# Kernel tuning notes

Hardware: AMD Instinct MI355X
Metric: run time of the kernel (lower is better)

## Reference

```python
import jax, jax.numpy as jnp
import numpy as np

N_NODES = 50000
N_EDGES = 400000
NODE_DIM = 128
NUM_BASIS = 20
MUL0, MUL1, MUL2 = 128, 64, 32          # 128x0e + 64x1e + 32x2e
NUM_IRREPS = MUL0 + MUL1 + MUL2         # 224
SPH_DIM = MUL0 + 3 * MUL1 + 5 * MUL2    # 480
HIDDEN = NODE_DIM + NUM_IRREPS          # 352
EPS = 1e-5


def layer_norm(x, g, b):
    mu = x.mean(-1, keepdims=True)
    var = ((x - mu) ** 2).mean(-1, keepdims=True)
    return (x - mu) * jax.lax.rsqrt(var + EPS) * g + b


def o3_layer_norm(x, w, b):
    # Equivariant layer norm per irrep block (Equiformer-style, component normalization).
    s = x[:, :MUL0]                                    # l=0 scalars [N,128]
    v = x[:, MUL0:MUL0 + 3 * MUL1].reshape(-1, MUL1, 3)  # l=1 [N,64,3]
    t = x[:, MUL0 + 3 * MUL1:].reshape(-1, MUL2, 5)      # l=2 [N,32,5]
    s = s - s.mean(-1, keepdims=True)
    s = s * jax.lax.rsqrt((s ** 2).mean(-1, keepdims=True) + EPS) * w[:MUL0] + b
    nv = (v ** 2).mean(axis=(-1, -2))[:, None, None]
    v = v * jax.lax.rsqrt(nv + EPS) * w[MUL0:MUL0 + MUL1][None, :, None]
    nt = (t ** 2).mean(axis=(-1, -2))[:, None, None]
    t = t * jax.lax.rsqrt(nt + EPS) * w[MUL0 + MUL1:][None, :, None]
    return jnp.concatenate([s, v.reshape(-1, 3 * MUL1), t.reshape(-1, 5 * MUL2)], axis=-1)


def sph_harm(vec):
    # e3nn spherical harmonics (normalize=True, normalization='component') up to l=2.
    u = vec * jax.lax.rsqrt((vec ** 2).sum(-1, keepdims=True))
    x, y, z = u[:, 0], u[:, 1], u[:, 2]
    s15 = np.float32(np.sqrt(15.0))
    s5 = np.float32(np.sqrt(5.0))
    sh1 = np.float32(np.sqrt(3.0)) * u  # [E,3]
    sh2 = jnp.stack([s15 * x * z,
                     s15 * x * y,
                     s5 * (y * y - 0.5 * (x * x + z * z)),
                     s15 * y * z,
                     0.5 * s15 * (z * z - x * x)], axis=-1)  # [E,5]
    return sh1, sh2


def _forward(x_scalar, x_spherical, rbf, vec, W1, b1, W2, b2, Wrbf, ln_g, ln_b, o3_w, o3_b, edge_index):
    dst, src = edge_index[0], edge_index[1]
    scalar_in = layer_norm(x_scalar, ln_g, ln_b)          # [N,128]
    spherical_in = o3_layer_norm(x_spherical, o3_w, o3_b)  # [N,480]
    h = jax.nn.silu(scalar_in @ W1 + b1)
    scalar_out = h @ W2 + b2                               # [N,352]
    filter_weight = rbf @ Wrbf                             # [E,352]
    filter_out = scalar_out[src] * filter_weight           # gather + elementwise [E,352]
    gate = filter_out[:, :NUM_IRREPS]                      # [E,224]
    message_scalar = filter_out[:, NUM_IRREPS:]            # [E,128]
    sh1, sh2 = sph_harm(vec)
    g0 = gate[:, :MUL0]
    g1 = gate[:, MUL0:MUL0 + MUL1]
    g2 = gate[:, MUL0 + MUL1:]
    # ElementwiseTensorProduct(edge_irreps, '224x0e'): scalar gate per irrep; l=0 SH == 1.
    msg1 = (g1[:, :, None] * sh1[:, None, :]).reshape(-1, 3 * MUL1)
    msg2 = (g2[:, :, None] * sh2[:, None, :]).reshape(-1, 5 * MUL2)
    message_spherical = jnp.concatenate([g0, msg1, msg2], axis=-1)  # [E,480]
    new_scalar = scalar_in.at[dst].add(message_scalar)
    new_spherical = spherical_in.at[dst].add(message_spherical)
    return new_scalar, new_spherical


def setup_inputs() -> dict:
    key = jax.random.key(0)
    ks = jax.random.split(key, 8)
    return {
        "x_scalar": jax.random.normal(ks[0], (N_NODES, NODE_DIM), dtype=jnp.float32),
        "x_spherical": jax.random.normal(ks[1], (N_NODES, SPH_DIM), dtype=jnp.float32),
        "rbf": jax.random.normal(ks[2], (N_EDGES, NUM_BASIS), dtype=jnp.float32),
        "vec": jax.random.normal(ks[3], (N_EDGES, 3), dtype=jnp.float32),
        "W1": jax.random.normal(ks[4], (NODE_DIM, NODE_DIM), dtype=jnp.float32) * 0.05,
        "b1": jnp.zeros((NODE_DIM,), jnp.float32),
        "W2": jax.random.normal(ks[5], (NODE_DIM, HIDDEN), dtype=jnp.float32) * 0.05,
        "b2": jnp.zeros((HIDDEN,), jnp.float32),
        "Wrbf": jax.random.normal(ks[6], (NUM_BASIS, HIDDEN), dtype=jnp.float32) * 0.05,
        "ln_g": jnp.ones((NODE_DIM,), jnp.float32),
        "ln_b": jnp.zeros((NODE_DIM,), jnp.float32),
        "o3_w": jnp.ones((NUM_IRREPS,), jnp.float32),
        "o3_b": jnp.zeros((MUL0,), jnp.float32),
        "edge_index": jax.random.randint(ks[7], (2, N_EDGES), 0, N_NODES),
    }


def reference(x_scalar, x_spherical, rbf, vec, W1, b1, W2, b2, Wrbf, ln_g, ln_b, o3_w, o3_b, edge_index):
    return _forward(x_scalar, x_spherical, rbf, vec, W1, b1, W2, b2, Wrbf, ln_g, ln_b, o3_w, o3_b, edge_index)
```

## Files before the change

### kernel.cpp

```cpp
#include <hip/hip_runtime.h>
#include <hip/hip_bf16.h>

#define N_DIM   128
#define MUL0    128
#define MUL1    64
#define MUL2    32
#define NIRR    224
#define SPHD    480
#define HID     352
#define NBASIS  20
#define EPSV    1e-5f

typedef __attribute__((ext_vector_type(8))) short bf16x8;
typedef __attribute__((ext_vector_type(4))) float f32x4;

__device__ __forceinline__ float wave_sum(float v) {
  #pragma unroll
  for (int o = 32; o > 0; o >>= 1) v += __shfl_xor(v, o, 64);
  return v;
}

__device__ __forceinline__ unsigned short f2bf(float f) {
  unsigned int u = __float_as_uint(f);
  u = (u + 0x7fff + ((u >> 16) & 1)) >> 16;
  return (unsigned short)u;
}

__global__ __launch_bounds__(256) void node_norm_kernel(
    const float* __restrict__ x_scalar, const float* __restrict__ x_sph,
    const float* __restrict__ ln_g, const float* __restrict__ ln_b,
    const float* __restrict__ o3_w, const float* __restrict__ o3_b,
    float* __restrict__ out_scal, float* __restrict__ out_sph, int n_nodes) {
  const int n = blockIdx.x * 4 + (threadIdx.x >> 6);
  if (n >= n_nodes) return;
  const int l = threadIdx.x & 63;

  const float* xs = x_scalar + (size_t)n * N_DIM;
  float a0 = xs[l], a1 = xs[l + 64];
  float mu = wave_sum(a0 + a1) * (1.f / 128.f);
  float d0 = a0 - mu, d1 = a1 - mu;
  float var = wave_sum(d0 * d0 + d1 * d1) * (1.f / 128.f);
  float sc = rsqrtf(var + EPSV);
  float* os = out_scal + (size_t)n * N_DIM;
  os[l]      = d0 * sc * ln_g[l]      + ln_b[l];
  os[l + 64] = d1 * sc * ln_g[l + 64] + ln_b[l + 64];

  const float* xp = x_sph + (size_t)n * SPHD;
  float s0 = xp[l], s1 = xp[l + 64];
  mu = wave_sum(s0 + s1) * (1.f / 128.f);
  d0 = s0 - mu; d1 = s1 - mu;
  var = wave_sum(d0 * d0 + d1 * d1) * (1.f / 128.f);
  sc = rsqrtf(var + EPSV);
  float* op = out_sph + (size_t)n * SPHD;
  op[l]      = d0 * sc * o3_w[l]      + o3_b[l];
  op[l + 64] = d1 * sc * o3_w[l + 64] + o3_b[l + 64];

  float v0 = xp[128 + l], v1 = xp[128 + 64 + l], v2 = xp[128 + 128 + l];
  float nv = wave_sum(v0 * v0 + v1 * v1 + v2 * v2) * (1.f / 192.f);
  sc = rsqrtf(nv + EPSV);
  op[128 + l]       = v0 * sc * o3_w[MUL0 + (l) / 3];
  op[128 + 64 + l]  = v1 * sc * o3_w[MUL0 + (l + 64) / 3];
  op[128 + 128 + l] = v2 * sc * o3_w[MUL0 + (l + 128) / 3];

  float t0 = xp[320 + l], t1 = xp[320 + 64 + l];
  float t2 = (l < 32) ? xp[320 + 128 + l] : 0.f;
  float nt = wave_sum(t0 * t0 + t1 * t1 + t2 * t2) * (1.f / 160.f);
  sc = rsqrtf(nt + EPSV);
  op[320 + l]      = t0 * sc * o3_w[MUL0 + MUL1 + (l) / 5];
  op[320 + 64 + l] = t1 * sc * o3_w[MUL0 + MUL1 + (l + 64) / 5];
  if (l < 32) op[320 + 128 + l] = t2 * sc * o3_w[MUL0 + MUL1 + (l + 128) / 5];
}

__global__ void pack_b_kernel(const float* __restrict__ B, unsigned short* __restrict__ Bp,
                              int N, int NT) {
  int id = blockIdx.x * 256 + threadIdx.x;
  int total = 4 * NT * 64;
  if (id >= total) return;
  int lane = id & 63;
  int tmp = id >> 6;
  int nt = tmp % NT, ks = tmp / NT;
  int n = nt * 16 + (lane & 15);
  int kb = ks * 32 + (lane >> 4) * 8;
  unsigned short* o = Bp + (size_t)id * 8;
  #pragma unroll
  for (int j = 0; j < 8; ++j)
    o[j] = (n < N) ? f2bf(B[(size_t)(kb + j) * N + n]) : (unsigned short)0;
}

template <bool A_BF16, bool SILU, bool OUT_BF16>
__global__ __launch_bounds__(256) void mfma_gemm_kernel(
    const void* __restrict__ Ap, const unsigned short* __restrict__ Bp,
    const float* __restrict__ bias, void* __restrict__ Cp,
    int M, int N, int NT) {
  const int lane = threadIdx.x & 63;
  const int wave = threadIdx.x >> 6;
  const int bm = blockIdx.x * 64 + wave * 16;
  const int bn = blockIdx.y * 64;
  const int q = lane >> 4;
  const int arow = min(bm + (lane & 15), M - 1);

  f32x4 acc[4] = {};
  #pragma unroll
  for (int ks = 0; ks < 4; ++ks) {
    const int k = ks * 32 + q * 8;
    bf16x8 a;
    if (A_BF16) {
      a = *(const bf16x8*)((const unsigned short*)Ap + (size_t)arow * 128 + k);
    } else {
      const float* ap = (const float*)Ap + (size_t)arow * 128 + k;
      float4 f0 = *(const float4*)ap;
      float4 f1 = *(const float4*)(ap + 4);
      union { bf16x8 v; unsigned short s[8]; } cv;
      cv.s[0] = f2bf(f0.x); cv.s[1] = f2bf(f0.y); cv.s[2] = f2bf(f0.z); cv.s[3] = f2bf(f0.w);
      cv.s[4] = f2bf(f1.x); cv.s[5] = f2bf(f1.y); cv.s[6] = f2bf(f1.z); cv.s[7] = f2bf(f1.w);
      a = cv.v;
    }
    #pragma unroll
    for (int nt = 0; nt < 4; ++nt) {
      bf16x8 b = *(const bf16x8*)(Bp + ((size_t)(ks * NT + blockIdx.y * 4 + nt) * 64 + lane) * 8);
      acc[nt] = __builtin_amdgcn_mfma_f32_16x16x32_bf16(a, b, acc[nt], 0, 0, 0);
    }
  }
  #pragma unroll
  for (int nt = 0; nt < 4; ++nt) {
    int col = bn + nt * 16 + (lane & 15);
    if (col >= N) continue;
    float bz = bias[col];
    #pragma unroll
    for (int i = 0; i < 4; ++i) {
      int r = bm + q * 4 + i;
      if (r >= M) continue;
      float v = acc[nt][i] + bz;
      if (SILU) v = v / (1.f + __expf(-v));
      if (OUT_BF16) ((unsigned short*)Cp)[(size_t)r * N + col] = f2bf(v);
      else          ((float*)Cp)[(size_t)r * N + col] = v;
    }
  }
}

__global__ void hist_kernel(const int* __restrict__ ei, int* __restrict__ deg, int n_edges) {
  int e = blockIdx.x * blockDim.x + threadIdx.x;
  if (e < n_edges) atomicAdd(&deg[ei[e]], 1);
}

__global__ __launch_bounds__(1024) void scan_part_kernel(
    const int* __restrict__ deg, int* __restrict__ offs, int* __restrict__ bsum, int n) {
  __shared__ int wsum[16];
  const int tid = threadIdx.x, lane = tid & 63, wid = tid >> 6;
  int i = blockIdx.x * 1024 + tid;
  int v = (i < n) ? deg[i] : 0;
  int s = v;
  #pragma unroll
  for (int o = 1; o < 64; o <<= 1) {
    int t = __shfl_up(s, o, 64);
    if (lane >= o) s += t;
  }
  if (lane == 63) wsum[wid] = s;
  __syncthreads();
  if (wid == 0) {
    int ws = (lane < 16) ? wsum[lane] : 0;
    #pragma unroll
    for (int o = 1; o < 16; o <<= 1) {
      int t = __shfl_up(ws, o, 64);
      if (lane >= o) ws += t;
    }
    if (lane < 16) wsum[lane] = ws;
  }
  __syncthreads();
  int excl = ((wid == 0) ? 0 : wsum[wid - 1]) + s - v;
  if (i < n) offs[i] = excl;
  if (tid == 1023) bsum[blockIdx.x] = wsum[15];
}

__global__ __launch_bounds__(64) void scan_tops_kernel(
    const int* __restrict__ bsum, int* __restrict__ bbase, int* __restrict__ offs,
    int nb, int n) {
  const int lane = threadIdx.x;
  int v = (lane < nb) ? bsum[lane] : 0;
  int s = v;
  #pragma unroll
  for (int o = 1; o < 64; o <<= 1) {
    int t = __shfl_up(s, o, 64);
    if (lane >= o) s += t;
  }
  if (lane < nb) bbase[lane] = s - v;
  if (lane == 63) offs[n] = s;
}

__global__ __launch_bounds__(1024) void scan_add_kernel(
    int* __restrict__ offs, const int* __restrict__ bbase, int n) {
  int i = blockIdx.x * 1024 + threadIdx.x;
  if (i < n) offs[i] += bbase[blockIdx.x];
}

__global__ void fill_kernel(const int* __restrict__ ei, const int* __restrict__ offs,
                            int* __restrict__ cursor, const int* __restrict__ edge_src,
                            const float* __restrict__ rbf, const float* __restrict__ vec,
                            float* __restrict__ rbf_s, float* __restrict__ vec_s,
                            int* __restrict__ src_s, int n_edges) {
  int e = blockIdx.x * blockDim.x + threadIdx.x;
  if (e < n_edges) {
    int d = ei[e];
    int p = atomicAdd(&cursor[d], 1);
    int ii = offs[d] + p;
    src_s[ii] = edge_src[e];
    const float4* rp = (const float4*)(rbf + (size_t)e * NBASIS);
    float4* op = (float4*)(rbf_s + (size_t)ii * NBASIS);
    op[0] = rp[0]; op[1] = rp[1]; op[2] = rp[2]; op[3] = rp[3]; op[4] = rp[4];
    vec_s[(size_t)ii * 3]     = vec[(size_t)e * 3];
    vec_s[(size_t)ii * 3 + 1] = vec[(size_t)e * 3 + 1];
    vec_s[(size_t)ii * 3 + 2] = vec[(size_t)e * 3 + 2];
  }
}

#define NPB 4
#define S3f  1.7320508075688772f
#define S15f 3.872983346207417f
#define S5f  2.2360679774997896f

__device__ __forceinline__ void edge_accum(
    int ii, float sA, float sB,
    const float* __restrict__ rbf_s, const float* __restrict__ vec_s,
    const float* wA, const float* wB, int t, bool hasB,
    float& a0, float& a1, float& a2, float& a3, float& a4, float& aB) {
  const float4* rp = (const float4*)(rbf_s + (size_t)ii * NBASIS);
  float4 r0 = rp[0], r1 = rp[1], r2 = rp[2], r3 = rp[3], r4 = rp[4];
  float rb[NBASIS] = {r0.x, r0.y, r0.z, r0.w, r1.x, r1.y, r1.z, r1.w,
                      r2.x, r2.y, r2.z, r2.w, r3.x, r3.y, r3.z, r3.w,
                      r4.x, r4.y, r4.z, r4.w};
  float fwA = 0.f;
  #pragma unroll
  for (int k = 0; k < NBASIS; ++k) fwA += rb[k] * wA[k];
  float fA = sA * fwA;

  if (t < 128) {
    a0 += fA;
  } else if (t < 224) {
    float vx = vec_s[3 * (size_t)ii], vy = vec_s[3 * (size_t)ii + 1], vz = vec_s[3 * (size_t)ii + 2];
    float rn = rsqrtf(vx * vx + vy * vy + vz * vz);
    float x = vx * rn, y = vy * rn, z = vz * rn;
    if (t < 192) {
      a0 += fA * (S3f * x); a1 += fA * (S3f * y); a2 += fA * (S3f * z);
    } else {
      a0 += fA * (S15f * x * z);
      a1 += fA * (S15f * x * y);
      a2 += fA * (S5f * (y * y - 0.5f * (x * x + z * z)));
      a3 += fA * (S15f * y * z);
      a4 += fA * (0.5f * S15f * (z * z - x * x));
    }
  } else {
    a0 += fA;
  }

  if (hasB) {
    float fwB = 0.f;
    #pragma unroll
    for (int k = 0; k < NBASIS; ++k) fwB += rb[k] * wB[k];
    aB += sB * fwB;
  }
}

__global__ __launch_bounds__(256) void gather_kernel(
    const float* __restrict__ rbf_s, const float* __restrict__ vec_s,
    const float* __restrict__ Wrbf, const float* __restrict__ so,
    const int* __restrict__ src_s, const int* __restrict__ offs,
    float* __restrict__ out_scal, float* __restrict__ out_sph, int n_nodes) {
  const int t = threadIdx.x;
  const bool hasB = (t < 96);
  const int cA = t;
  const int cB = hasB ? (256 + t) : 256;

  float wA[NBASIS], wB[NBASIS];
  #pragma unroll
  for (int k = 0; k < NBASIS; ++k) {
    wA[k] = Wrbf[k * HID + cA];
    wB[k] = Wrbf[k * HID + cB];
  }

  const int nb = blockIdx.x * NPB;
  for (int nn = 0; nn < NPB; ++nn) {
    const int node = nb + nn;
    if (node >= n_nodes) break;
    float a0 = 0.f, a1 = 0.f, a2 = 0.f, a3 = 0.f, a4 = 0.f, aB = 0.f;
    const int e0 = offs[node], e1 = offs[node + 1];

    int ii = e0;
    for (; ii + 4 <= e1; ii += 4) {
      const int s0 = src_s[ii], s1 = src_s[ii + 1], s2 = src_s[ii + 2], s3 = src_s[ii + 3];
      const float* p0 = so + (size_t)s0 * HID;
      const float* p1 = so + (size_t)s1 * HID;
      const float* p2 = so + (size_t)s2 * HID;
      const float* p3 = so + (size_t)s3 * HID;
      float sA0 = p0[cA], sA1 = p1[cA], sA2 = p2[cA], sA3 = p3[cA];
      float sB0 = hasB ? p0[cB] : 0.f;
      float sB1 = hasB ? p1[cB] : 0.f;
      float sB2 = hasB ? p2[cB] : 0.f;
      float sB3 = hasB ? p3[cB] : 0.f;
      edge_accum(ii,     sA0, sB0, rbf_s, vec_s, wA, wB, t, hasB, a0, a1, a2, a3, a4, aB);
      edge_accum(ii + 1, sA1, sB1, rbf_s, vec_s, wA, wB, t, hasB, a0, a1, a2, a3, a4, aB);
      edge_accum(ii + 2, sA2, sB2, rbf_s, vec_s, wA, wB, t, hasB, a0, a1, a2, a3, a4, aB);
      edge_accum(ii + 3, sA3, sB3, rbf_s, vec_s, wA, wB, t, hasB, a0, a1, a2, a3, a4, aB);
    }
    for (; ii + 2 <= e1; ii += 2) {
      const int s0 = src_s[ii], s1 = src_s[ii + 1];
      const float* p0 = so + (size_t)s0 * HID;
      const float* p1 = so + (size_t)s1 * HID;
      float sA0 = p0[cA], sA1 = p1[cA];
      float sB0 = hasB ? p0[cB] : 0.f;
      float sB1 = hasB ? p1[cB] : 0.f;
      edge_accum(ii,     sA0, sB0, rbf_s, vec_s, wA, wB, t, hasB, a0, a1, a2, a3, a4, aB);
      edge_accum(ii + 1, sA1, sB1, rbf_s, vec_s, wA, wB, t, hasB, a0, a1, a2, a3, a4, aB);
    }
    if (ii < e1) {
      const int s0 = src_s[ii];
      const float* p0 = so + (size_t)s0 * HID;
      float sA0 = p0[cA];
      float sB0 = hasB ? p0[cB] : 0.f;
      edge_accum(ii, sA0, sB0, rbf_s, vec_s, wA, wB, t, hasB, a0, a1, a2, a3, a4, aB);
    }

    float* sph = out_sph + (size_t)node * SPHD;
    float* scl = out_scal + (size_t)node * N_DIM;
    if (t < 128) {
      sph[t] += a0;
    } else if (t < 192) {
      float* p = sph + 128 + 3 * (t - 128);
      p[0] += a0; p[1] += a1; p[2] += a2;
    } else if (t < 224) {
      float* p = sph + 320 + 5 * (t - 192);
      p[0] += a0; p[1] += a1; p[2] += a2; p[3] += a3; p[4] += a4;
    } else {
      scl[t - 224] += a0;
    }
    if (hasB) scl[t + 32] += aB;
  }
}

extern "C" void kernel_launch(void* const* d_in, const int* in_sizes, int n_in,
                              void* d_out, int out_size, void* d_ws, size_t ws_size,
                              hipStream_t stream) {
  const float* x_scalar = (const float*)d_in[0];
  const float* x_sph    = (const float*)d_in[1];
  const float* rbf      = (const float*)d_in[2];
  const float* vec      = (const float*)d_in[3];
  const float* W1       = (const float*)d_in[4];
  const float* b1       = (const float*)d_in[5];
  const float* W2       = (const float*)d_in[6];
  const float* b2       = (const float*)d_in[7];
  const float* Wrbf     = (const float*)d_in[8];
  const float* ln_g     = (const float*)d_in[9];
  const float* ln_b     = (const float*)d_in[10];
  const float* o3_w     = (const float*)d_in[11];
  const float* o3_b     = (const float*)d_in[12];
  const int*   edge_idx = (const int*)d_in[13];

  const int n_nodes = in_sizes[0] / N_DIM;
  const int n_edges = in_sizes[2] / NBASIS;

  float* out_scal = (float*)d_out;
  float* out_sph  = out_scal + (size_t)n_nodes * N_DIM;

  float* rbf_s = (float*)d_ws;
  float* vec_s = rbf_s + (size_t)n_edges * NBASIS;
  int*   src_s = (int*)(vec_s + (size_t)n_edges * 3);
  float* ws_so = (float*)(src_s + n_edges);
  unsigned short* h_bf = (unsigned short*)(ws_so + (size_t)n_nodes * HID);
  unsigned short* bp1  = h_bf + (size_t)n_nodes * N_DIM;
  unsigned short* bp2  = bp1 + 16384;
  int* deg    = (int*)(bp2 + 49152);
  int* cursor = deg + n_nodes;
  int* offs   = cursor + n_nodes;
  int* bsum   = offs + n_nodes + 1;
  int* bbase  = bsum + 64;

  const int* edge_dst = edge_idx;
  const int* edge_src = edge_idx + n_edges;

  node_norm_kernel<<<(n_nodes + 3) / 4, 256, 0, stream>>>(
      x_scalar, x_sph, ln_g, ln_b, o3_w, o3_b, out_scal, out_sph, n_nodes);

  pack_b_kernel<<<8, 256, 0, stream>>>(W1, bp1, N_DIM, 8);
  pack_b_kernel<<<24, 256, 0, stream>>>(W2, bp2, HID, 24);

  {
    dim3 g((n_nodes + 63) / 64, 2);
    mfma_gemm_kernel<false, true, true><<<g, 256, 0, stream>>>(
        out_scal, bp1, b1, h_bf, n_nodes, N_DIM, 8);
  }
  {
    dim3 g((n_nodes + 63) / 64, 6);
    mfma_gemm_kernel<true, false, false><<<g, 256, 0, stream>>>(
        h_bf, bp2, b2, ws_so, n_nodes, HID, 24);
  }

  hipMemsetAsync(deg, 0, sizeof(int) * 2 * n_nodes, stream);
  hist_kernel<<<(n_edges + 255) / 256, 256, 0, stream>>>(edge_dst, deg, n_edges);
  const int nb = (n_nodes + 1023) / 1024;
  scan_part_kernel<<<nb, 1024, 0, stream>>>(deg, offs, bsum, n_nodes);
  scan_tops_kernel<<<1, 64, 0, stream>>>(bsum, bbase, offs, nb, n_nodes);
  scan_add_kernel<<<nb, 1024, 0, stream>>>(offs, bbase, n_nodes);
  fill_kernel<<<(n_edges + 255) / 256, 256, 0, stream>>>(
      edge_dst, offs, cursor, edge_src, rbf, vec, rbf_s, vec_s, src_s, n_edges);

  gather_kernel<<<(n_nodes + NPB - 1) / NPB, 256, 0, stream>>>(
      rbf_s, vec_s, Wrbf, ws_so, src_s, offs, out_scal, out_sph, n_nodes);
}
```

Before: 676.4 us.

## Store scalar_out in bf16 with interleaved column layout for gather

```diff
diff --git a/kernel.cpp b/kernel.cpp
--- a/kernel.cpp
+++ b/kernel.cpp
@@ -24,6 +24,10 @@
   unsigned int u = __float_as_uint(f);
   u = (u + 0x7fff + ((u >> 16) & 1)) >> 16;
   return (unsigned short)u;
+}
+
+__device__ __forceinline__ float bf2f(unsigned short v) {
+  return __uint_as_float(((unsigned int)v) << 16);
 }
 
 __global__ __launch_bounds__(256) void node_norm_kernel(
@@ -87,7 +91,7 @@
     o[j] = (n < N) ? f2bf(B[(size_t)(kb + j) * N + n]) : (unsigned short)0;
 }
 
-template <bool A_BF16, bool SILU, bool OUT_BF16>
+template <bool A_BF16, bool SILU, bool OUT_BF16, bool PERM>
 __global__ __launch_bounds__(256) void mfma_gemm_kernel(
     const void* __restrict__ Ap, const unsigned short* __restrict__ Bp,
     const float* __restrict__ bias, void* __restrict__ Cp,
@@ -126,14 +130,16 @@
     int col = bn + nt * 16 + (lane & 15);
     if (col >= N) continue;
     float bz = bias[col];
+    int pcol = col;
+    if (PERM) pcol = (col < 96) ? (2 * col) : ((col < 256) ? (col + 96) : (2 * (col - 256) + 1));
     #pragma unroll
     for (int i = 0; i < 4; ++i) {
       int r = bm + q * 4 + i;
       if (r >= M) continue;
       float v = acc[nt][i] + bz;
       if (SILU) v = v / (1.f + __expf(-v));
-      if (OUT_BF16) ((unsigned short*)Cp)[(size_t)r * N + col] = f2bf(v);
-      else          ((float*)Cp)[(size_t)r * N + col] = v;
+      if (OUT_BF16) ((unsigned short*)Cp)[(size_t)r * N + pcol] = f2bf(v);
+      else          ((float*)Cp)[(size_t)r * N + pcol] = v;
     }
   }
 }
@@ -218,6 +224,20 @@
 #define S15f 3.872983346207417f
 #define S5f  2.2360679774997896f
 
+__device__ __forceinline__ void so_load(const unsigned short* __restrict__ so,
+                                        int src, int t, bool hasB,
+                                        float& sA, float& sB) {
+  const unsigned short* p = so + (size_t)src * HID;
+  if (hasB) {
+    unsigned int u = *(const unsigned int*)(p + 2 * t);
+    sA = __uint_as_float(u << 16);
+    sB = __uint_as_float(u & 0xffff0000u);
+  } else {
+    sA = bf2f(p[t + 96]);
+    sB = 0.f;
+  }
+}
+
 __device__ __forceinline__ void edge_accum(
     int ii, float sA, float sB,
     const float* __restrict__ rbf_s, const float* __restrict__ vec_s,
@@ -262,7 +282,7 @@
 
 __global__ __launch_bounds__(256) void gather_kernel(
     const float* __restrict__ rbf_s, const float* __restrict__ vec_s,
-    const float* __restrict__ Wrbf, const float* __restrict__ so,
+    const float* __restrict__ Wrbf, const unsigned short* __restrict__ so,
     const int* __restrict__ src_s, const int* __restrict__ offs,
     float* __restrict__ out_scal, float* __restrict__ out_sph, int n_nodes) {
   const int t = threadIdx.x;
@@ -287,15 +307,11 @@
     int ii = e0;
     for (; ii + 4 <= e1; ii += 4) {
       const int s0 = src_s[ii], s1 = src_s[ii + 1], s2 = src_s[ii + 2], s3 = src_s[ii + 3];
-      const float* p0 = so + (size_t)s0 * HID;
-      const float* p1 = so + (size_t)s1 * HID;
-      const float* p2 = so + (size_t)s2 * HID;
-      const float* p3 = so + (size_t)s3 * HID;
-      float sA0 = p0[cA], sA1 = p1[cA], sA2 = p2[cA], sA3 = p3[cA];
-      float sB0 = hasB ? p0[cB] : 0.f;
-      float sB1 = hasB ? p1[cB] : 0.f;
-      float sB2 = hasB ? p2[cB] : 0.f;
-      float sB3 = hasB ? p3[cB] : 0.f;
+      float sA0, sB0, sA1, sB1, sA2, sB2, sA3, sB3;
+      so_load(so, s0, t, hasB, sA0, sB0);
+      so_load(so, s1, t, hasB, sA1, sB1);
+      so_load(so, s2, t, hasB, sA2, sB2);
+      so_load(so, s3, t, hasB, sA3, sB3);
       edge_accum(ii,     sA0, sB0, rbf_s, vec_s, wA, wB, t, hasB, a0, a1, a2, a3, a4, aB);
       edge_accum(ii + 1, sA1, sB1, rbf_s, vec_s, wA, wB, t, hasB, a0, a1, a2, a3, a4, aB);
       edge_accum(ii + 2, sA2, sB2, rbf_s, vec_s, wA, wB, t, hasB, a0, a1, a2, a3, a4, aB);
@@ -303,19 +319,16 @@
     }
     for (; ii + 2 <= e1; ii += 2) {
       const int s0 = src_s[ii], s1 = src_s[ii + 1];
-      const float* p0 = so + (size_t)s0 * HID;
-      const float* p1 = so + (size_t)s1 * HID;
-      float sA0 = p0[cA], sA1 = p1[cA];
-      float sB0 = hasB ? p0[cB] : 0.f;
-      float sB1 = hasB ? p1[cB] : 0.f;
+      float sA0, sB0, sA1, sB1;
+      so_load(so, s0, t, hasB, sA0, sB0);
+      so_load(so, s1, t, hasB, sA1, sB1);
       edge_accum(ii,     sA0, sB0, rbf_s, vec_s, wA, wB, t, hasB, a0, a1, a2, a3, a4, aB);
       edge_accum(ii + 1, sA1, sB1, rbf_s, vec_s, wA, wB, t, hasB, a0, a1, a2, a3, a4, aB);
     }
     if (ii < e1) {
       const int s0 = src_s[ii];
-      const float* p0 = so + (size_t)s0 * HID;
-      float sA0 = p0[cA];
-      float sB0 = hasB ? p0[cB] : 0.f;
+      float sA0, sB0;
+      so_load(so, s0, t, hasB, sA0, sB0);
       edge_accum(ii, sA0, sB0, rbf_s, vec_s, wA, wB, t, hasB, a0, a1, a2, a3, a4, aB);
     }
 
@@ -363,10 +376,10 @@
   float* rbf_s = (float*)d_ws;
   float* vec_s = rbf_s + (size_t)n_edges * NBASIS;
   int*   src_s = (int*)(vec_s + (size_t)n_edges * 3);
-  float* ws_so = (float*)(src_s + n_edges);
-  unsigned short* h_bf = (unsigned short*)(ws_so + (size_t)n_nodes * HID);
-  unsigned short* bp1  = h_bf + (size_t)n_nodes * N_DIM;
-  unsigned short* bp2  = bp1 + 16384;
+  unsigned short* so_bf = (unsigned short*)(src_s + n_edges);
+  unsigned short* h_bf  = so_bf + (size_t)n_nodes * HID;
+  unsigned short* bp1   = h_bf + (size_t)n_nodes * N_DIM;
+  unsigned short* bp2   = bp1 + 16384;
   int* deg    = (int*)(bp2 + 49152);
   int* cursor = deg + n_nodes;
   int* offs   = cursor + n_nodes;
@@ -384,13 +397,13 @@
 
   {
     dim3 g((n_nodes + 63) / 64, 2);
-    mfma_gemm_kernel<false, true, true><<<g, 256, 0, stream>>>(
+    mfma_gemm_kernel<false, true, true, false><<<g, 256, 0, stream>>>(
         out_scal, bp1, b1, h_bf, n_nodes, N_DIM, 8);
   }
   {
     dim3 g((n_nodes + 63) / 64, 6);
-    mfma_gemm_kernel<true, false, false><<<g, 256, 0, stream>>>(
-        h_bf, bp2, b2, ws_so, n_nodes, HID, 24);
+    mfma_gemm_kernel<true, false, true, true><<<g, 256, 0, stream>>>(
+        h_bf, bp2, b2, so_bf, n_nodes, HID, 24);
   }
 
   hipMemsetAsync(deg, 0, sizeof(int) * 2 * n_nodes, stream);
@@ -403,5 +416,5 @@
       edge_dst, offs, cursor, edge_src, rbf, vec, rbf_s, vec_s, src_s, n_edges);
 
   gather_kernel<<<(n_nodes + NPB - 1) / NPB, 256, 0, stream>>>(
-      rbf_s, vec_s, Wrbf, ws_so, src_s, offs, out_scal, out_sph, n_nodes);
-}
+      rbf_s, vec_s, Wrbf, so_bf, src_s, offs, out_scal, out_sph, n_nodes);
+}
```

Measured after the change: 679.8 us. About the same (+0.5%).
